# Performance work log

Measured on AMD Instinct MI355X. Metric: run time of the kernel, lower is better.

## Reference

```python
import jax, jax.numpy as jnp
import numpy as np

N_NODES = 100000
N_REL = 4
N_EDGES = 400000
IN_F, H_F, OUT_F = 128, 128, 64


def setup_inputs() -> dict:
    key = jax.random.key(0)
    ks = jax.random.split(key, 7)
    x = jax.random.normal(ks[0], (N_NODES, IN_F), dtype=jnp.float32)
    src_idx = jax.random.randint(ks[1], (N_REL, N_EDGES), 0, N_NODES, dtype=jnp.int64)
    dst_idx = jax.random.randint(ks[2], (N_REL, N_EDGES), 0, N_NODES, dtype=jnp.int64)
    # Glorot-ish scale for the per-relation GraphConv weights
    W1 = jax.random.normal(ks[3], (N_REL, IN_F, H_F), dtype=jnp.float32) * (1.0 / np.sqrt(IN_F))
    b1 = jnp.zeros((N_REL, H_F), dtype=jnp.float32)
    W2 = jax.random.normal(ks[4], (N_REL, H_F, OUT_F), dtype=jnp.float32) * (1.0 / np.sqrt(H_F))
    b2 = jnp.zeros((N_REL, OUT_F), dtype=jnp.float32)
    return {"x": x, "src_idx": src_idx, "dst_idx": dst_idx,
            "W1": W1, "b1": b1, "W2": W2, "b2": b2}


def _graph_conv(x, src, dst, W, b):
    """DGL GraphConv with norm='both': out = D_in^{-1/2} A^T D_out^{-1/2} x W + b."""
    n = x.shape[0]
    ones = jnp.ones(src.shape[0], dtype=x.dtype)
    deg_out = jnp.maximum(jax.ops.segment_sum(ones, src, num_segments=n), 1.0)
    deg_in = jnp.maximum(jax.ops.segment_sum(ones, dst, num_segments=n), 1.0)
    xn = x * jax.lax.rsqrt(deg_out)[:, None]              # [N, F] src-side norm
    msg = jnp.take(xn, src, axis=0)                        # [E, F] gather
    agg = jax.ops.segment_sum(msg, dst, num_segments=n)   # [N, F] scatter-add
    agg = agg * jax.lax.rsqrt(deg_in)[:, None]            # dst-side norm
    return agg @ W + b


def _hetero_layer(x, src_idx, dst_idx, Ws, bs):
    # per-relation conv, sum-aggregated across relations (HeteroGraphConv 'sum')
    per_rel = jax.vmap(lambda s, d, W, b: _graph_conv(x, s, d, W, b))(src_idx, dst_idx, Ws, bs)
    return per_rel.sum(axis=0)


def reference(x, src_idx, dst_idx, W1, b1, W2, b2):
    h = jax.nn.relu(_hetero_layer(x, src_idx, dst_idx, W1, b1))
    return _hetero_layer(h, src_idx, dst_idx, W2, b2)
```

## Files before the change

### kernel.cpp

```cpp
#include <hip/hip_runtime.h>
#include <hip/hip_bf16.h>

#define NN 100000
#define NR 4
#define NE 400000
#define INF 128
#define HF 128
#define OUTF 64

#define WIN 16384
#define WIN2 (WIN / 2)
#define NWIN 7
#define SUB 16
#define SLICE (NE / SUB)

typedef __attribute__((ext_vector_type(8))) short s16x8;
typedef __attribute__((ext_vector_type(4))) float f32x4;

__global__ __launch_bounds__(256) void deg_win_kernel(const int* __restrict__ src,
                                                      const int* __restrict__ dst,
                                                      unsigned int* __restrict__ parts) {
    __shared__ unsigned int hist[WIN2];
    int arr = blockIdx.z;
    int r   = blockIdx.y;
    int win = blockIdx.x / SUB;
    int sub = blockIdx.x % SUB;
    const int4* idx4 = (const int4*)((arr ? dst : src) + (size_t)r * NE + (size_t)sub * SLICE);
    int base = win * WIN;

    uint4 z4 = make_uint4(0, 0, 0, 0);
    for (int i = threadIdx.x; i < WIN2 / 4; i += 256) ((uint4*)hist)[i] = z4;
    __syncthreads();

    auto proc = [&](int4 v) {
        int a;
        a = v.x - base; if ((unsigned)a < WIN) atomicAdd(&hist[a >> 1], 1u << ((a & 1) << 4));
        a = v.y - base; if ((unsigned)a < WIN) atomicAdd(&hist[a >> 1], 1u << ((a & 1) << 4));
        a = v.z - base; if ((unsigned)a < WIN) atomicAdd(&hist[a >> 1], 1u << ((a & 1) << 4));
        a = v.w - base; if ((unsigned)a < WIN) atomicAdd(&hist[a >> 1], 1u << ((a & 1) << 4));
    };

    constexpr int NV = SLICE / 4;
    int i = threadIdx.x;
    for (; i + 256 < NV; i += 512) {
        int4 va = idx4[i];
        int4 vb = idx4[i + 256];
        proc(va);
        proc(vb);
    }
    if (i < NV) proc(idx4[i]);
    __syncthreads();

    unsigned int* outp = parts + ((((size_t)arr * NR + r) * NWIN + win) * SUB + sub) * WIN2;
    for (int j = threadIdx.x; j < WIN2 / 4; j += 256)
        ((uint4*)outp)[j] = ((const uint4*)hist)[j];
}

__global__ void red_norm_kernel(const unsigned int* __restrict__ parts, int* __restrict__ deg_tot,
                                float* __restrict__ rno, float* __restrict__ rni) {
    int n = blockIdx.x * blockDim.x + threadIdx.x;
    if (n >= NN) return;
    if (n == 0) deg_tot[NN] = 0;
    int win = n / WIN, off = n % WIN;
    int word = off >> 1, sh = (off & 1) << 4;
    int tot = 0;
    #pragma unroll
    for (int r = 0; r < NR; r++) {
        const unsigned int* p0 = parts + (((size_t)0 * NR + r) * NWIN + win) * SUB * WIN2 + word;
        const unsigned int* p1 = parts + (((size_t)1 * NR + r) * NWIN + win) * SUB * WIN2 + word;
        int so = 0, si = 0;
        #pragma unroll
        for (int s = 0; s < SUB; s++) {
            so += (p0[(size_t)s * WIN2] >> sh) & 0xFFFFu;
            si += (p1[(size_t)s * WIN2] >> sh) & 0xFFFFu;
        }
        rno[(size_t)r * NN + n] = rsqrtf(fmaxf((float)so, 1.0f));
        rni[(size_t)r * NN + n] = rsqrtf(fmaxf((float)si, 1.0f));
        tot += si;
    }
    deg_tot[n] = tot;
}

__global__ void scan_block_kernel(const int* __restrict__ in, int* __restrict__ out,
                                  int* __restrict__ blockSums, int n) {
    __shared__ int sd[256];
    int t = threadIdx.x;
    int base = blockIdx.x * 1024 + t * 4;
    int v[4];
    #pragma unroll
    for (int j = 0; j < 4; j++) v[j] = (base + j < n) ? ((in[base + j] + 7) & ~7) : 0;
    int ts = v[0] + v[1] + v[2] + v[3];
    sd[t] = ts;
    __syncthreads();
    int acc = ts;
    for (int off = 1; off < 256; off <<= 1) {
        int x = (t >= off) ? sd[t - off] : 0;
        __syncthreads();
        acc += x; sd[t] = acc;
        __syncthreads();
    }
    int run = acc - ts;
    #pragma unroll
    for (int j = 0; j < 4; j++) {
        if (base + j < n) out[base + j] = run;
        run += v[j];
    }
    if (t == 255) blockSums[blockIdx.x] = acc;
}

__global__ void scan_sums_kernel(int* __restrict__ blockSums, int nb) {
    __shared__ int sd[512];
    int t = threadIdx.x;
    int v = (t < nb) ? blockSums[t] : 0;
    sd[t] = v;
    __syncthreads();
    int acc = v;
    for (int off = 1; off < 512; off <<= 1) {
        int x = (t >= off) ? sd[t - off] : 0;
        __syncthreads();
        acc += x; sd[t] = acc;
        __syncthreads();
    }
    if (t < nb) blockSums[t] = acc - v;
}

__global__ void scan_add_kernel(int* __restrict__ row_ptr, const int* __restrict__ blockSums,
                                int* __restrict__ cursor, int n) {
    int i = blockIdx.x * blockDim.x + threadIdx.x;
    if (i < n) {
        int v = row_ptr[i] + blockSums[i >> 10];
        row_ptr[i] = v;
        if (i < NN) cursor[i] = v;
    }
}

__global__ void pad_fill_kernel(const int* __restrict__ row_ptr, const int* __restrict__ deg_tot,
                                int2* __restrict__ edges) {
    int n = blockIdx.x * blockDim.x + threadIdx.x;
    if (n >= NN) return;
    int b = row_ptr[n] + deg_tot[n];
    int e = row_ptr[n + 1];
    for (int i = b; i < e; i++) edges[i] = make_int2(0, 0);
}

__global__ void csr_build_kernel(const int* __restrict__ src, const int* __restrict__ dst,
                                 const float* __restrict__ rno, const float* __restrict__ rni,
                                 int* __restrict__ cursor, int2* __restrict__ edges) {
    int r = blockIdx.y;
    int i = blockIdx.x * blockDim.x + threadIdx.x;
    if (i >= NE) return;
    int s = src[(size_t)r * NE + i];
    int d = dst[(size_t)r * NE + i];
    int pos = atomicAdd(&cursor[d], 1);
    float c = rno[(size_t)r * NN + s] * rni[(size_t)r * NN + d];
    edges[pos] = make_int2((r * NN + s) << 8, __float_as_int(c));
}

__global__ void prep_kernel(const float* __restrict__ W1, const float* __restrict__ W2,
                            const float* __restrict__ b1, const float* __restrict__ b2,
                            __hip_bfloat16* __restrict__ Wt1, __hip_bfloat16* __restrict__ Wt2,
                            float* __restrict__ bsum1, float* __restrict__ bsum2) {
    if (blockIdx.x == 384) {
        int t = threadIdx.x;
        if (t < HF) {
            float s = 0.f;
            for (int r = 0; r < NR; r++) s += b1[r * HF + t];
            bsum1[t] = s;
        } else if (t < HF + OUTF) {
            int f = t - HF;
            float s = 0.f;
            for (int r = 0; r < NR; r++) s += b2[r * OUTF + f];
            bsum2[f] = s;
        }
        return;
    }
    int id = blockIdx.x * 256 + threadIdx.x;
    if (id < NR * HF * INF) {
        int r = id >> 14, rem = id & 16383;
        int n_ = rem >> 7, k = rem & 127;
        Wt1[id] = __float2bfloat16(W1[((size_t)r * INF + k) * HF + n_]);
    } else {
        int id2 = id - NR * HF * INF;
        if (id2 < NR * OUTF * HF) {
            int r = id2 >> 13, rem = id2 & 8191;
            int n_ = rem >> 7, k = rem & 127;
            Wt2[id2] = __float2bfloat16(W2[((size_t)r * HF + k) * OUTF + n_]);
        }
    }
}

__device__ __forceinline__ s16x8 pack_bf16x8(float4 a0, float4 a1) {
    union { s16x8 v; __hip_bfloat162 h[4]; } u;
    u.h[0] = __float22bfloat162_rn(make_float2(a0.x, a0.y));
    u.h[1] = __float22bfloat162_rn(make_float2(a0.z, a0.w));
    u.h[2] = __float22bfloat162_rn(make_float2(a1.x, a1.y));
    u.h[3] = __float22bfloat162_rn(make_float2(a1.z, a1.w));
    return u.v;
}

__device__ __forceinline__ void load_lds_16(const void* g, void* l) {
    __builtin_amdgcn_global_load_lds(
        (const __attribute__((address_space(1))) void*)g,
        (__attribute__((address_space(3))) void*)l, 16, 0, 0);
}

template<int F, typename AT>
__global__ __launch_bounds__(256, 3) void gemm_all(const AT* __restrict__ Xb,
                                                   const __hip_bfloat16* __restrict__ Wt,
                                                   __hip_bfloat16* __restrict__ Zb, int nrel) {
    constexpr int NT = F / 16;
    constexpr int NG = F * 16;
    __shared__ __attribute__((aligned(16))) __hip_bfloat16 Bs[F * 128];

    int tid  = threadIdx.x;
    int wid  = tid >> 6;
    int lane = tid & 63;
    int quad = lane >> 4;
    int l16  = lane & 15;
    int sw   = l16 & 7;

    int mbase = blockIdx.x * 128;

    int bofs[4];
    #pragma unroll
    for (int kb = 0; kb < 4; kb++)
        bofs[kb] = l16 * 256 + (((kb * 4 + quad) ^ sw) << 4);

    s16x8 afr[2][4];
    #pragma unroll
    for (int mt = 0; mt < 2; mt++) {
        int mrow = mbase + mt * 64 + wid * 16 + l16;
        if (mrow >= NN) mrow = NN - 1;
        #pragma unroll
        for (int kb = 0; kb < 4; kb++) {
            if constexpr (sizeof(AT) == 4) {
                const float* xr = (const float*)Xb + (size_t)mrow * 128 + kb * 32 + quad * 8;
                float4 a0 = *(const float4*)xr;
                float4 a1 = *(const float4*)(xr + 4);
                afr[mt][kb] = pack_bf16x8(a0, a1);
            } else {
                afr[mt][kb] = *(const s16x8*)((const __hip_bfloat16*)Xb + (size_t)mrow * 128 + kb * 32 + quad * 8);
            }
        }
    }

    for (int rel = 0; rel < nrel; rel++) {
        if (rel) __syncthreads();

        {
            const char* W = (const char*)(Wt + (size_t)rel * F * 128);
            #pragma unroll
            for (int it = 0; it < NG / 256; it++) {
                int dg = it * 256 + tid;
                int sg = dg ^ ((dg >> 4) & 7);
                load_lds_16(W + (size_t)sg * 16, (char*)Bs + (size_t)(dg & ~63) * 16);
            }
        }
        __syncthreads();

        __hip_bfloat16* Z = Zb + (size_t)rel * NN * F;

        f32x4 acc[2][NT];
        #pragma unroll
        for (int nt = 0; nt < NT; nt++) {
            acc[0][nt] = (f32x4){0.f, 0.f, 0.f, 0.f};
            acc[1][nt] = (f32x4){0.f, 0.f, 0.f, 0.f};
            #pragma unroll
            for (int kb = 0; kb < 4; kb++) {
                s16x8 bfr = *(const s16x8*)((const char*)Bs + nt * 4096 + bofs[kb]);
                acc[0][nt] = __builtin_amdgcn_mfma_f32_16x16x32_bf16(bfr, afr[0][kb], acc[0][nt], 0, 0, 0);
                acc[1][nt] = __builtin_amdgcn_mfma_f32_16x16x32_bf16(bfr, afr[1][kb], acc[1][nt], 0, 0, 0);
            }
        }

        #pragma unroll
        for (int mt = 0; mt < 2; mt++) {
            int g = mbase + mt * 64 + wid * 16 + l16;
            if (g < NN) {
                #pragma unroll
                for (int nt = 0; nt < NT; nt++) {
                    union { uint2 u; __hip_bfloat162 h[2]; } o;
                    o.h[0] = __float22bfloat162_rn(make_float2(acc[mt][nt][0], acc[mt][nt][1]));
                    o.h[1] = __float22bfloat162_rn(make_float2(acc[mt][nt][2], acc[mt][nt][3]));
                    *(uint2*)(Z + (size_t)g * F + nt * 16 + quad * 4) = o.u;
                }
            }
        }
    }
}

template<int F, bool RELU, bool OUT_F32>
__global__ __launch_bounds__(256) void gather_merged(const int* __restrict__ row_ptr,
                              const int2* __restrict__ edges,
                              const __hip_bfloat16* __restrict__ Zb,
                              float* __restrict__ outf, __hip_bfloat16* __restrict__ outb,
                              const float* __restrict__ bsum) {
    int wid  = threadIdx.x >> 6;
    int lane = threadIdx.x & 63;
    int n = blockIdx.x * 4 + wid;
    int beg = row_ptr[n];
    int end = row_ptr[n + 1];

    if constexpr (F == 128) {
        const char* Zl = (const char*)Zb + lane * 4;
        float2 a = *(const float2*)(bsum + lane * 2);
        for (int p = beg; p < end; p += 8) {
            int2 e[8];
            #pragma unroll
            for (int j = 0; j < 8; j++) e[j] = edges[p + j];
            float2 zz[8];
            #pragma unroll
            for (int j = 0; j < 8; j++)
                zz[j] = __bfloat1622float2(*(const __hip_bfloat162*)(Zl + e[j].x));
            #pragma unroll
            for (int j = 0; j < 8; j++) {
                float c = __int_as_float(e[j].y);
                a.x = fmaf(c, zz[j].x, a.x);
                a.y = fmaf(c, zz[j].y, a.y);
            }
        }
        if constexpr (RELU) { a.x = fmaxf(a.x, 0.f); a.y = fmaxf(a.y, 0.f); }
        *(__hip_bfloat162*)(outb + (size_t)n * 128 + lane * 2) = __float22bfloat162_rn(a);
    } else {
        const char* Zl = (const char*)Zb + lane * 2;
        float a = bsum[lane];
        for (int p = beg; p < end; p += 8) {
            int2 e[8];
            #pragma unroll
            for (int j = 0; j < 8; j++) e[j] = edges[p + j];
            float zz[8];
            #pragma unroll
            for (int j = 0; j < 8; j++)
                zz[j] = __bfloat162float(*(const __hip_bfloat16*)(Zl + (e[j].x >> 1)));
            #pragma unroll
            for (int j = 0; j < 8; j++) a = fmaf(__int_as_float(e[j].y), zz[j], a);
        }
        if constexpr (RELU) a = fmaxf(a, 0.f);
        if constexpr (OUT_F32) outf[(size_t)n * 64 + lane] = a;
        else outb[(size_t)n * 64 + lane] = __float2bfloat16(a);
    }
}

extern "C" void kernel_launch(void* const* d_in, const int* in_sizes, int n_in,
                              void* d_out, int out_size, void* d_ws, size_t ws_size,
                              hipStream_t stream) {
    const float* x   = (const float*)d_in[0];
    const int*   src = (const int*)  d_in[1];
    const int*   dst = (const int*)  d_in[2];
    const float* W1  = (const float*)d_in[3];
    const float* b1  = (const float*)d_in[4];
    const float* W2  = (const float*)d_in[5];
    const float* b2  = (const float*)d_in[6];
    float* out = (float*)d_out;

    constexpr int RN = NR * NN;
    constexpr int NSC = NN + 1;
    constexpr int NB = (NSC + 1023) / 1024;

    char* p = (char*)d_ws;
    int*   deg_tot   = (int*)p;   p += ((size_t)NN + 16) * 4;
    float* rno       = (float*)p; p += (size_t)RN * 4;
    float* rni       = (float*)p; p += (size_t)RN * 4;
    int*   row_ptr   = (int*)p;   p += ((size_t)NN + 16) * 4;
    int*   cursor    = (int*)p;   p += (size_t)NN * 4;
    int*   blockSums = (int*)p;   p += 1024 * 4;
    int2*  edges     = (int2*)p;  p += ((size_t)NR * NE + 8 * NN) * 8;
    float* bsum1 = (float*)p; p += HF * 4;
    float* bsum2 = (float*)p; p += OUTF * 4;
    __hip_bfloat16* hb  = (__hip_bfloat16*)p; p += (size_t)NN * HF * 2;
    __hip_bfloat16* Wt1 = (__hip_bfloat16*)p; p += (size_t)NR * HF * INF * 2;
    __hip_bfloat16* Wt2 = (__hip_bfloat16*)p; p += (size_t)NR * OUTF * HF * 2;
    __hip_bfloat16* Zb = (__hip_bfloat16*)p;
    unsigned int* parts = (unsigned int*)Zb;

    prep_kernel<<<385, 256, 0, stream>>>(W1, W2, b1, b2, Wt1, Wt2, bsum1, bsum2);
    deg_win_kernel<<<dim3(NWIN * SUB, NR, 2), 256, 0, stream>>>(src, dst, parts);
    red_norm_kernel<<<(NN + 255) / 256, 256, 0, stream>>>(parts, deg_tot, rno, rni);
    scan_block_kernel<<<NB, 256, 0, stream>>>(deg_tot, row_ptr, blockSums, NSC);
    scan_sums_kernel<<<1, 512, 0, stream>>>(blockSums, NB);
    scan_add_kernel<<<(NSC + 255) / 256, 256, 0, stream>>>(row_ptr, blockSums, cursor, NSC);
    pad_fill_kernel<<<(NN + 255) / 256, 256, 0, stream>>>(row_ptr, deg_tot, edges);
    csr_build_kernel<<<dim3((NE + 255) / 256, NR), 256, 0, stream>>>(
        src, dst, rno, rni, cursor, edges);

    constexpr int GB = (NN + 127) / 128;
    constexpr int GG = NN / 4;

    gemm_all<HF, float><<<GB, 256, 0, stream>>>(x, Wt1, Zb, 4);
    gather_merged<HF, true, false><<<GG, 256, 0, stream>>>(
        row_ptr, edges, Zb, nullptr, hb, bsum1);

    gemm_all<OUTF, __hip_bfloat16><<<GB, 256, 0, stream>>>(hb, Wt2, Zb, 4);
    gather_merged<OUTF, false, true><<<GG, 256, 0, stream>>>(
        row_ptr, edges, Zb, out, nullptr, bsum2);
}
```

Baseline: 400.2 us.

## Partition CSR build by destination window to localize atomics and scattered writes

The CSR build kernel now launches 512 blocks, each owning one of 8 destination-node windows for one relation and one edge slice. Each block scans its slice with int4 loads and handles only edges whose destination falls in its window. Cursor atomics, rni reads and edge writes therefore land in a smaller address range, which should improve L2 locality. The cost is that every edge index is read 8 times, with 7 of the 8 reads discarded, and the grid has fewer blocks.

Result: slower. 419.6 us (+4.8%).

```diff
diff --git a/kernel.cpp b/kernel.cpp
--- a/kernel.cpp
+++ b/kernel.cpp
@@ -13,6 +13,8 @@
 #define NWIN 7
 #define SUB 16
 #define SLICE (NE / SUB)
+
+#define WCS 12500
 
 typedef __attribute__((ext_vector_type(8))) short s16x8;
 typedef __attribute__((ext_vector_type(4))) float f32x4;
@@ -143,17 +145,37 @@
     for (int i = b; i < e; i++) edges[i] = make_int2(0, 0);
 }
 
-__global__ void csr_build_kernel(const int* __restrict__ src, const int* __restrict__ dst,
+__global__ __launch_bounds__(256) void csr_build_kernel(const int* __restrict__ src,
+                                 const int* __restrict__ dst,
                                  const float* __restrict__ rno, const float* __restrict__ rni,
                                  int* __restrict__ cursor, int2* __restrict__ edges) {
-    int r = blockIdx.y;
-    int i = blockIdx.x * blockDim.x + threadIdx.x;
-    if (i >= NE) return;
-    int s = src[(size_t)r * NE + i];
-    int d = dst[(size_t)r * NE + i];
-    int pos = atomicAdd(&cursor[d], 1);
-    float c = rno[(size_t)r * NN + s] * rni[(size_t)r * NN + d];
-    edges[pos] = make_int2((r * NN + s) << 8, __float_as_int(c));
+    int b   = blockIdx.x;
+    int w   = b & 7;
+    int k   = b >> 3;
+    int r   = k >> 4;
+    int sub = k & 15;
+    int base = w * WCS;
+
+    const int4* sp4 = (const int4*)(src + (size_t)r * NE + (size_t)sub * SLICE);
+    const int4* dp4 = (const int4*)(dst + (size_t)r * NE + (size_t)sub * SLICE);
+
+    auto one = [&](int s, int d) {
+        if ((unsigned)(d - base) < WCS) {
+            int pos = atomicAdd(&cursor[d], 1);
+            float c = rno[(size_t)r * NN + s] * rni[(size_t)r * NN + d];
+            edges[pos] = make_int2((r * NN + s) << 8, __float_as_int(c));
+        }
+    };
+
+    constexpr int NV = SLICE / 4;
+    for (int i = threadIdx.x; i < NV; i += 256) {
+        int4 d4 = dp4[i];
+        int4 s4 = sp4[i];
+        one(s4.x, d4.x);
+        one(s4.y, d4.y);
+        one(s4.z, d4.z);
+        one(s4.w, d4.w);
+    }
 }
 
 __global__ void prep_kernel(const float* __restrict__ W1, const float* __restrict__ W2,
@@ -380,8 +402,7 @@
     scan_sums_kernel<<<1, 512, 0, stream>>>(blockSums, NB);
     scan_add_kernel<<<(NSC + 255) / 256, 256, 0, stream>>>(row_ptr, blockSums, cursor, NSC);
     pad_fill_kernel<<<(NN + 255) / 256, 256, 0, stream>>>(row_ptr, deg_tot, edges);
-    csr_build_kernel<<<dim3((NE + 255) / 256, NR), 256, 0, stream>>>(
-        src, dst, rno, rni, cursor, edges);
+    csr_build_kernel<<<512, 256, 0, stream>>>(src, dst, rno, rni, cursor, edges);
 
     constexpr int GB = (NN + 127) / 128;
     constexpr int GG = NN / 4;
```

## Fuse CSR build, pad fill and layer-1 GEMM into one interleaved launch

Applied to the files above, without the earlier changes.

Merges the CSR edge scatter, the padding fill and the first-layer per-relation GEMM into a single kernel. Blocks are interleaved so every third block runs a GEMM tile and the others run CSR-build or pad work. The intent is to overlap the atomic- and memory-bound CSR construction with the compute-bound GEMM and to save two kernel launches. In exchange, every block reserves the GEMM's 32KB of shared memory, which can limit occupancy for the lightweight CSR blocks, and the block-index mapping becomes harder to follow.

After: 367.9 us. 1.09x faster.

```diff
diff --git a/kernel.cpp b/kernel.cpp
--- a/kernel.cpp
+++ b/kernel.cpp
@@ -13,6 +13,12 @@
 #define NWIN 7
 #define SUB 16
 #define SLICE (NE / SUB)
+
+#define GB 782
+#define CB 1563
+#define CSRB (NR * CB)
+#define PADB 391
+#define FGRID (GB + CSRB + PADB)
 
 typedef __attribute__((ext_vector_type(8))) short s16x8;
 typedef __attribute__((ext_vector_type(4))) float f32x4;
@@ -134,28 +140,6 @@
     }
 }
 
-__global__ void pad_fill_kernel(const int* __restrict__ row_ptr, const int* __restrict__ deg_tot,
-                                int2* __restrict__ edges) {
-    int n = blockIdx.x * blockDim.x + threadIdx.x;
-    if (n >= NN) return;
-    int b = row_ptr[n] + deg_tot[n];
-    int e = row_ptr[n + 1];
-    for (int i = b; i < e; i++) edges[i] = make_int2(0, 0);
-}
-
-__global__ void csr_build_kernel(const int* __restrict__ src, const int* __restrict__ dst,
-                                 const float* __restrict__ rno, const float* __restrict__ rni,
-                                 int* __restrict__ cursor, int2* __restrict__ edges) {
-    int r = blockIdx.y;
-    int i = blockIdx.x * blockDim.x + threadIdx.x;
-    if (i >= NE) return;
-    int s = src[(size_t)r * NE + i];
-    int d = dst[(size_t)r * NE + i];
-    int pos = atomicAdd(&cursor[d], 1);
-    float c = rno[(size_t)r * NN + s] * rni[(size_t)r * NN + d];
-    edges[pos] = make_int2((r * NN + s) << 8, __float_as_int(c));
-}
-
 __global__ void prep_kernel(const float* __restrict__ W1, const float* __restrict__ W2,
                             const float* __restrict__ b1, const float* __restrict__ b2,
                             __hip_bfloat16* __restrict__ Wt1, __hip_bfloat16* __restrict__ Wt2,
@@ -205,12 +189,12 @@
 }
 
 template<int F, typename AT>
-__global__ __launch_bounds__(256, 3) void gemm_all(const AT* __restrict__ Xb,
-                                                   const __hip_bfloat16* __restrict__ Wt,
-                                                   __hip_bfloat16* __restrict__ Zb, int nrel) {
+__device__ __forceinline__ void gemm_body(int mbase, const AT* __restrict__ Xb,
+                                          const __hip_bfloat16* __restrict__ Wt,
+                                          __hip_bfloat16* __restrict__ Zb, int nrel,
+                                          __hip_bfloat16* Bs) {
     constexpr int NT = F / 16;
     constexpr int NG = F * 16;
-    __shared__ __attribute__((aligned(16))) __hip_bfloat16 Bs[F * 128];
 
     int tid  = threadIdx.x;
     int wid  = tid >> 6;
@@ -218,8 +202,6 @@
     int quad = lane >> 4;
     int l16  = lane & 15;
     int sw   = l16 & 7;
-
-    int mbase = blockIdx.x * 128;
 
     int bofs[4];
     #pragma unroll
@@ -289,6 +271,51 @@
     }
 }
 
+__global__ __launch_bounds__(256, 3) void fused1_kernel(
+        const float* __restrict__ x, const __hip_bfloat16* __restrict__ Wt1,
+        __hip_bfloat16* __restrict__ Zb,
+        const int* __restrict__ src, const int* __restrict__ dst,
+        const float* __restrict__ rno, const float* __restrict__ rni,
+        int* __restrict__ cursor, int2* __restrict__ edges,
+        const int* __restrict__ row_ptr, const int* __restrict__ deg_tot) {
+    __shared__ __attribute__((aligned(16))) __hip_bfloat16 Bs[HF * 128];
+    int b = blockIdx.x;
+    bool isg = (b % 3 == 1) && (b / 3 < GB);
+    if (isg) {
+        gemm_body<HF, float>((b / 3) * 128, x, Wt1, Zb, NR, Bs);
+        return;
+    }
+    int cnt = (b <= 1) ? 0 : ((b + 1) / 3);
+    if (cnt > GB) cnt = GB;
+    int ng = b - cnt;
+    if (ng < CSRB) {
+        int r = ng / CB;
+        int i = (ng % CB) * 256 + threadIdx.x;
+        if (i < NE) {
+            int s = src[(size_t)r * NE + i];
+            int d = dst[(size_t)r * NE + i];
+            int pos = atomicAdd(&cursor[d], 1);
+            float c = rno[(size_t)r * NN + s] * rni[(size_t)r * NN + d];
+            edges[pos] = make_int2((r * NN + s) << 8, __float_as_int(c));
+        }
+    } else {
+        int n = (ng - CSRB) * 256 + threadIdx.x;
+        if (n < NN) {
+            int pb = row_ptr[n] + deg_tot[n];
+            int pe = row_ptr[n + 1];
+            for (int i = pb; i < pe; i++) edges[i] = make_int2(0, 0);
+        }
+    }
+}
+
+template<int F, typename AT>
+__global__ __launch_bounds__(256, 3) void gemm_all(const AT* __restrict__ Xb,
+                                                   const __hip_bfloat16* __restrict__ Wt,
+                                                   __hip_bfloat16* __restrict__ Zb, int nrel) {
+    __shared__ __attribute__((aligned(16))) __hip_bfloat16 Bs[F * 128];
+    gemm_body<F, AT>(blockIdx.x * 128, Xb, Wt, Zb, nrel, Bs);
+}
+
 template<int F, bool RELU, bool OUT_F32>
 __global__ __launch_bounds__(256) void gather_merged(const int* __restrict__ row_ptr,
                               const int2* __restrict__ edges,
@@ -379,14 +406,12 @@
     scan_block_kernel<<<NB, 256, 0, stream>>>(deg_tot, row_ptr, blockSums, NSC);
     scan_sums_kernel<<<1, 512, 0, stream>>>(blockSums, NB);
     scan_add_kernel<<<(NSC + 255) / 256, 256, 0, stream>>>(row_ptr, blockSums, cursor, NSC);
-    pad_fill_kernel<<<(NN + 255) / 256, 256, 0, stream>>>(row_ptr, deg_tot, edges);
-    csr_build_kernel<<<dim3((NE + 255) / 256, NR), 256, 0, stream>>>(
-        src, dst, rno, rni, cursor, edges);
-
-    constexpr int GB = (NN + 127) / 128;
+
+    fused1_kernel<<<FGRID, 256, 0, stream>>>(x, Wt1, Zb, src, dst, rno, rni,
+                                             cursor, edges, row_ptr, deg_tot);
+
     constexpr int GG = NN / 4;
 
-    gemm_all<HF, float><<<GB, 256, 0, stream>>>(x, Wt1, Zb, 4);
     gather_merged<HF, true, false><<<GG, 256, 0, stream>>>(
         row_ptr, edges, Zb, nullptr, hb, bsum1);
 
```
